# Optimization experiments

Hardware: AMD Instinct MI355X
Metric: run time of the kernel (lower is better)

Reference implementation:

```python
import jax, jax.numpy as jnp
import numpy as np

N_NODES = 50000
N_EDGES = 800000
IN_F = 32
HID = 64
N_LAYERS = 3
BN_EPS = 1e-5


def setup_inputs() -> dict:
    key = jax.random.key(0)
    ks = jax.random.split(key, 8)
    x = jax.random.normal(ks[0], (N_NODES, IN_F), dtype=jnp.float32)
    edge_index = jax.random.randint(ks[1], (2, N_EDGES), 0, N_NODES, dtype=jnp.int64)
    W_embed = jax.random.normal(ks[2], (IN_F, HID), dtype=jnp.float32) / np.sqrt(IN_F)
    b_embed = jnp.zeros((HID,), dtype=jnp.float32)
    W_convs = jax.random.normal(ks[3], (N_LAYERS, HID, HID), dtype=jnp.float32) / np.sqrt(HID)
    b_convs = jnp.zeros((N_LAYERS, HID), dtype=jnp.float32)
    bn_gamma = jnp.ones((HID,), dtype=jnp.float32)
    bn_beta = jnp.zeros((HID,), dtype=jnp.float32)
    return {"x": x, "edge_index": edge_index, "W_embed": W_embed, "b_embed": b_embed,
            "W_convs": W_convs, "b_convs": b_convs, "bn_gamma": bn_gamma, "bn_beta": bn_beta}


def _gcn_norm(edge_index, n_nodes):
    # PyG GCNConv: add self-loops, symmetric normalization deg^-1/2 * deg^-1/2
    loops = jnp.arange(n_nodes, dtype=edge_index.dtype)
    src = jnp.concatenate([edge_index[0], loops])
    dst = jnp.concatenate([edge_index[1], loops])
    deg = jax.ops.segment_sum(jnp.ones_like(dst, dtype=jnp.float32), dst, num_segments=n_nodes)
    dinv = jax.lax.rsqrt(jnp.maximum(deg, 1.0))
    norm = dinv[src] * dinv[dst]  # [E+N]
    return src, dst, norm


def reference(x, edge_index, W_embed, b_embed, W_convs, b_convs, bn_gamma, bn_beta):
    n = x.shape[0]
    src, dst, norm = _gcn_norm(edge_index, n)

    h = jax.nn.relu(x @ W_embed + b_embed)  # [N, HID]
    for l in range(N_LAYERS):
        res = h
        # GCNConv: linear transform, then normalized neighbor aggregation
        t = h @ W_convs[l] + b_convs[l]
        msg = t[src] * norm[:, None]                           # [E+N, HID]
        agg = jax.ops.segment_sum(msg, dst, num_segments=n)    # [N, HID]
        # BatchNorm1d (training-mode batch stats), shared across layers
        mu = jnp.mean(agg, axis=0)
        var = jnp.var(agg, axis=0)
        bn = (agg - mu) * jax.lax.rsqrt(var + BN_EPS) * bn_gamma + bn_beta
        h = jax.nn.relu(bn) + res
    return h
```

## Files before the change

kernel.cpp:

```cpp
#include <hip/hip_runtime.h>

#define IN_F 32
#define HID 64
#define N_LAYERS 3
#define BN_EPS 1e-5f

__device__ __forceinline__ unsigned short f2bf(float x) {
    unsigned u = __float_as_uint(x);
    u += 0x7fffu + ((u >> 16) & 1u);
    return (unsigned short)(u >> 16);
}
__device__ __forceinline__ float bflo(unsigned v) { return __uint_as_float(v << 16); }
__device__ __forceinline__ float bfhi(unsigned v) { return __uint_as_float(v & 0xffff0000u); }

__global__ __launch_bounds__(256) void k_zero(int* cnt, int* cursor, float* statsAll, int n) {
    int i = blockIdx.x * blockDim.x + threadIdx.x;
    if (i < n) cnt[i] = 0;
    if (i == 0) *cursor = 0;
    if (i < 2 * HID * N_LAYERS) statsAll[i] = 0.0f;
}

__global__ __launch_bounds__(256) void k_hist_rank(const int* __restrict__ dst, int* cnt,
                                                   unsigned short* __restrict__ rank, int e) {
    int i = blockIdx.x * blockDim.x + threadIdx.x;
    if (i >= e) return;
    int r = atomicAdd(&cnt[dst[i]], 1);
    rank[i] = (unsigned short)r;
}

__global__ __launch_bounds__(256) void k_assign(const int* __restrict__ cnt, int* rowbeg,
                                                float* dinv, int* cursor, int n) {
    int i = blockIdx.x * blockDim.x + threadIdx.x;
    int lane = threadIdx.x & 63;
    int c = (i < n) ? cnt[i] : 0;
    int s = c;
#pragma unroll
    for (int off = 1; off < 64; off <<= 1) {
        int t = __shfl_up(s, off, 64);
        if (lane >= off) s += t;
    }
    int total = __shfl(s, 63, 64);
    int base = 0;
    if (lane == 63) base = atomicAdd(cursor, total);
    base = __shfl(base, 63, 64);
    if (i < n) {
        rowbeg[i] = base + s - c;
        dinv[i] = rsqrtf((float)(c + 1));
    }
}

__global__ __launch_bounds__(256) void k_fill(const int* __restrict__ src,
                                              const int* __restrict__ dst,
                                              const int* __restrict__ rowbeg,
                                              const unsigned short* __restrict__ rank,
                                              unsigned short* __restrict__ csr_src, int e) {
    int i = blockIdx.x * blockDim.x + threadIdx.x;
    if (i >= e) return;
    int pos = rowbeg[dst[i]] + (int)rank[i];
    csr_src[pos] = (unsigned short)src[i];
}

__global__ __launch_bounds__(256) void k_embed_conv(const float* __restrict__ x,
                                                    const float* __restrict__ We,
                                                    const float* __restrict__ be,
                                                    const float* __restrict__ Wc,
                                                    const float* __restrict__ bc,
                                                    const float* __restrict__ dinv,
                                                    float* __restrict__ h,
                                                    unsigned short* __restrict__ t2b, int n) {
    __shared__ float sWe[IN_F * HID];
    __shared__ float sWc[HID * HID];
    __shared__ float sh[4][HID];
    for (int i = threadIdx.x; i < IN_F * HID; i += blockDim.x) sWe[i] = We[i];
    for (int i = threadIdx.x; i < HID * HID; i += blockDim.x) sWc[i] = Wc[i];
    __syncthreads();
    int f = threadIdx.x & 63;
    int wv = threadIdx.x >> 6;
    int plane = f >> 5, fin = f & 31;
    float bef = be[f], bcf = bc[f];
    int w0 = blockIdx.x * 4 + wv;
    int nw = gridDim.x * 4;
    for (int node = w0; node < n; node += nw) {
        const float* xr = x + (size_t)node * IN_F;
        float acc = bef;
#pragma unroll
        for (int k = 0; k < IN_F; ++k) acc = fmaf(xr[k], sWe[k * HID + f], acc);
        float hv = fmaxf(acc, 0.0f);
        h[(size_t)node * HID + f] = hv;
        sh[wv][f] = hv;
        float acc2 = bcf;
#pragma unroll
        for (int k4 = 0; k4 < HID / 4; ++k4) {
            float4 hv4 = ((const float4*)sh[wv])[k4];
            acc2 = fmaf(hv4.x, sWc[(k4 * 4 + 0) * HID + f], acc2);
            acc2 = fmaf(hv4.y, sWc[(k4 * 4 + 1) * HID + f], acc2);
            acc2 = fmaf(hv4.z, sWc[(k4 * 4 + 2) * HID + f], acc2);
            acc2 = fmaf(hv4.w, sWc[(k4 * 4 + 3) * HID + f], acc2);
        }
        t2b[(size_t)plane * n * 32 + (size_t)node * 32 + fin] = f2bf(acc2 * dinv[node]);
    }
}

__global__ __launch_bounds__(256) void k_bn_conv(const float* __restrict__ agg,
                                                 const float* __restrict__ stats,
                                                 const float* __restrict__ gamma,
                                                 const float* __restrict__ beta,
                                                 const float* __restrict__ W,
                                                 const float* __restrict__ b,
                                                 const float* __restrict__ dinv,
                                                 float* __restrict__ h,
                                                 unsigned short* __restrict__ t2b, int n, float invN) {
    __shared__ float sW[HID * HID];
    __shared__ float sh[4][HID];
    for (int i = threadIdx.x; i < HID * HID; i += blockDim.x) sW[i] = W[i];
    __syncthreads();
    int f = threadIdx.x & 63;
    int wv = threadIdx.x >> 6;
    int plane = f >> 5, fin = f & 31;
    float mu = stats[f] * invN;
    float var = fmaxf(stats[HID + f] * invN - mu * mu, 0.0f);
    float scale = rsqrtf(var + BN_EPS) * gamma[f];
    float shift = beta[f];
    float bf = b[f];
    int w0 = blockIdx.x * 4 + wv;
    int nw = gridDim.x * 4;
    for (int node = w0; node < n; node += nw) {
        size_t gid = (size_t)node * HID + f;
        float bnv = (agg[gid] - mu) * scale + shift;
        float hv = fmaxf(bnv, 0.0f) + h[gid];
        h[gid] = hv;
        sh[wv][f] = hv;
        float acc = bf;
#pragma unroll
        for (int k4 = 0; k4 < HID / 4; ++k4) {
            float4 hv4 = ((const float4*)sh[wv])[k4];
            acc = fmaf(hv4.x, sW[(k4 * 4 + 0) * HID + f], acc);
            acc = fmaf(hv4.y, sW[(k4 * 4 + 1) * HID + f], acc);
            acc = fmaf(hv4.z, sW[(k4 * 4 + 2) * HID + f], acc);
            acc = fmaf(hv4.w, sW[(k4 * 4 + 3) * HID + f], acc);
        }
        t2b[(size_t)plane * n * 32 + (size_t)node * 32 + fin] = f2bf(acc * dinv[node]);
    }
}

__global__ __launch_bounds__(256) void k_aggregate(const int* __restrict__ rowbeg,
                                                   const int* __restrict__ cnt,
                                                   const unsigned short* __restrict__ csr_src,
                                                   const unsigned short* __restrict__ t2b,
                                                   const float* __restrict__ dinv,
                                                   float* __restrict__ agg,
                                                   float* __restrict__ stats, int n) {
    __shared__ float lsum[HID], lsq[HID];
    if (threadIdx.x < HID) { lsum[threadIdx.x] = 0.0f; lsq[threadIdx.x] = 0.0f; }
    __syncthreads();

    const int plane = blockIdx.y;
    const unsigned short* tb = t2b + (size_t)plane * n * 32;

    int l4 = threadIdx.x & 3;
    int node = blockIdx.x * 64 + (threadIdx.x >> 2);

    float4 r0 = make_float4(0.f, 0.f, 0.f, 0.f);
    float4 r1 = make_float4(0.f, 0.f, 0.f, 0.f);

    if (node < n) {
        int beg = rowbeg[node], end = beg + cnt[node];
        uint4 sv = ((const uint4*)(tb + (size_t)node * 32))[l4];
        float4 a0, a1;
        a0.x = bflo(sv.x); a0.y = bfhi(sv.x); a0.z = bflo(sv.y); a0.w = bfhi(sv.y);
        a1.x = bflo(sv.z); a1.y = bfhi(sv.z); a1.z = bflo(sv.w); a1.w = bfhi(sv.w);
        int j = beg;
        for (; j + 8 <= end; j += 8) {
            int s0 = csr_src[j + 0], s1 = csr_src[j + 1];
            int s2 = csr_src[j + 2], s3 = csr_src[j + 3];
            int s4 = csr_src[j + 4], s5 = csr_src[j + 5];
            int s6 = csr_src[j + 6], s7 = csr_src[j + 7];
            uint4 v0 = ((const uint4*)(tb + (size_t)s0 * 32))[l4];
            uint4 v1 = ((const uint4*)(tb + (size_t)s1 * 32))[l4];
            uint4 v2 = ((const uint4*)(tb + (size_t)s2 * 32))[l4];
            uint4 v3 = ((const uint4*)(tb + (size_t)s3 * 32))[l4];
            uint4 v4 = ((const uint4*)(tb + (size_t)s4 * 32))[l4];
            uint4 v5 = ((const uint4*)(tb + (size_t)s5 * 32))[l4];
            uint4 v6 = ((const uint4*)(tb + (size_t)s6 * 32))[l4];
            uint4 v7 = ((const uint4*)(tb + (size_t)s7 * 32))[l4];
            a0.x += bflo(v0.x) + bflo(v1.x) + bflo(v2.x) + bflo(v3.x)
                  + bflo(v4.x) + bflo(v5.x) + bflo(v6.x) + bflo(v7.x);
            a0.y += bfhi(v0.x) + bfhi(v1.x) + bfhi(v2.x) + bfhi(v3.x)
                  + bfhi(v4.x) + bfhi(v5.x) + bfhi(v6.x) + bfhi(v7.x);
            a0.z += bflo(v0.y) + bflo(v1.y) + bflo(v2.y) + bflo(v3.y)
                  + bflo(v4.y) + bflo(v5.y) + bflo(v6.y) + bflo(v7.y);
            a0.w += bfhi(v0.y) + bfhi(v1.y) + bfhi(v2.y) + bfhi(v3.y)
                  + bfhi(v4.y) + bfhi(v5.y) + bfhi(v6.y) + bfhi(v7.y);
            a1.x += bflo(v0.z) + bflo(v1.z) + bflo(v2.z) + bflo(v3.z)
                  + bflo(v4.z) + bflo(v5.z) + bflo(v6.z) + bflo(v7.z);
            a1.y += bfhi(v0.z) + bfhi(v1.z) + bfhi(v2.z) + bfhi(v3.z)
                  + bfhi(v4.z) + bfhi(v5.z) + bfhi(v6.z) + bfhi(v7.z);
            a1.z += bflo(v0.w) + bflo(v1.w) + bflo(v2.w) + bflo(v3.w)
                  + bflo(v4.w) + bflo(v5.w) + bflo(v6.w) + bflo(v7.w);
            a1.w += bfhi(v0.w) + bfhi(v1.w) + bfhi(v2.w) + bfhi(v3.w)
                  + bfhi(v4.w) + bfhi(v5.w) + bfhi(v6.w) + bfhi(v7.w);
        }
        for (; j < end; ++j) {
            int s = csr_src[j];
            uint4 v = ((const uint4*)(tb + (size_t)s * 32))[l4];
            a0.x += bflo(v.x); a0.y += bfhi(v.x); a0.z += bflo(v.y); a0.w += bfhi(v.y);
            a1.x += bflo(v.z); a1.y += bfhi(v.z); a1.z += bflo(v.w); a1.w += bfhi(v.w);
        }
        float dv = dinv[node];
        r0.x = a0.x * dv; r0.y = a0.y * dv; r0.z = a0.z * dv; r0.w = a0.w * dv;
        r1.x = a1.x * dv; r1.y = a1.y * dv; r1.z = a1.z * dv; r1.w = a1.w * dv;
        float4* ar = (float4*)(agg + (size_t)node * HID + plane * 32);
        ar[l4 * 2 + 0] = r0;
        ar[l4 * 2 + 1] = r1;
    }

    float4 q0, q1;
    q0.x = r0.x * r0.x; q0.y = r0.y * r0.y; q0.z = r0.z * r0.z; q0.w = r0.w * r0.w;
    q1.x = r1.x * r1.x; q1.y = r1.y * r1.y; q1.z = r1.z * r1.z; q1.w = r1.w * r1.w;
#pragma unroll
    for (int off = 4; off < 64; off <<= 1) {
        r0.x += __shfl_xor(r0.x, off, 64); q0.x += __shfl_xor(q0.x, off, 64);
        r0.y += __shfl_xor(r0.y, off, 64); q0.y += __shfl_xor(q0.y, off, 64);
        r0.z += __shfl_xor(r0.z, off, 64); q0.z += __shfl_xor(q0.z, off, 64);
        r0.w += __shfl_xor(r0.w, off, 64); q0.w += __shfl_xor(q0.w, off, 64);
        r1.x += __shfl_xor(r1.x, off, 64); q1.x += __shfl_xor(q1.x, off, 64);
        r1.y += __shfl_xor(r1.y, off, 64); q1.y += __shfl_xor(q1.y, off, 64);
        r1.z += __shfl_xor(r1.z, off, 64); q1.z += __shfl_xor(q1.z, off, 64);
        r1.w += __shfl_xor(r1.w, off, 64); q1.w += __shfl_xor(q1.w, off, 64);
    }
    if ((threadIdx.x & 63) < 4) {
        int f0 = plane * 32 + l4 * 8;
        atomicAdd(&lsum[f0 + 0], r0.x); atomicAdd(&lsq[f0 + 0], q0.x);
        atomicAdd(&lsum[f0 + 1], r0.y); atomicAdd(&lsq[f0 + 1], q0.y);
        atomicAdd(&lsum[f0 + 2], r0.z); atomicAdd(&lsq[f0 + 2], q0.z);
        atomicAdd(&lsum[f0 + 3], r0.w); atomicAdd(&lsq[f0 + 3], q0.w);
        atomicAdd(&lsum[f0 + 4], r1.x); atomicAdd(&lsq[f0 + 4], q1.x);
        atomicAdd(&lsum[f0 + 5], r1.y); atomicAdd(&lsq[f0 + 5], q1.y);
        atomicAdd(&lsum[f0 + 6], r1.z); atomicAdd(&lsq[f0 + 6], q1.z);
        atomicAdd(&lsum[f0 + 7], r1.w); atomicAdd(&lsq[f0 + 7], q1.w);
    }
    __syncthreads();
    int fs = plane * 32 + (threadIdx.x & 31);
    if (threadIdx.x < 32) {
        atomicAdd(&stats[fs], lsum[fs]);
        atomicAdd(&stats[HID + fs], lsq[fs]);
    }
}

__global__ __launch_bounds__(256) void k_bn_apply(const float* __restrict__ agg,
                                                  const float* __restrict__ stats,
                                                  const float* __restrict__ gamma,
                                                  const float* __restrict__ beta,
                                                  float* __restrict__ h, int n, float invN) {
    int gid = blockIdx.x * blockDim.x + threadIdx.x;
    int node = gid >> 6, f = gid & 63;
    if (node >= n) return;
    float mu = stats[f] * invN;
    float var = fmaxf(stats[HID + f] * invN - mu * mu, 0.0f);
    float bn = (agg[gid] - mu) * rsqrtf(var + BN_EPS) * gamma[f] + beta[f];
    h[gid] = fmaxf(bn, 0.0f) + h[gid];
}

extern "C" void kernel_launch(void* const* d_in, const int* in_sizes, int n_in,
                              void* d_out, int out_size, void* d_ws, size_t ws_size,
                              hipStream_t stream) {
    const float* x       = (const float*)d_in[0];
    const int*   ei      = (const int*)d_in[1];
    const float* W_embed = (const float*)d_in[2];
    const float* b_embed = (const float*)d_in[3];
    const float* W_convs = (const float*)d_in[4];
    const float* b_convs = (const float*)d_in[5];
    const float* gamma   = (const float*)d_in[6];
    const float* beta    = (const float*)d_in[7];
    float* h = (float*)d_out;

    const int n = in_sizes[0] / IN_F;
    const int e = in_sizes[1] / 2;
    const int* src = ei;
    const int* dst = ei + e;

    unsigned short* t2b = (unsigned short*)d_ws;
    float* agg      = (float*)(t2b + (size_t)n * HID);
    float* dinv     = agg + (size_t)n * HID;
    float* statsAll = dinv + n;
    int*   rowbeg   = (int*)(statsAll + 2 * HID * N_LAYERS);
    int*   cnt      = rowbeg + n;
    int*   cursor   = cnt + n;
    unsigned short* csr_src = (unsigned short*)(cursor + 1);
    unsigned short* rank    = csr_src + e;

    const int nodeBlocks  = (n + 255) / 256;
    const int nfBlocks    = (n * HID + 255) / 256;
    const int edgeBlocks  = (e + 255) / 256;
    const dim3 aggGrid((n + 63) / 64, 2);
    const int embedBlocks = 1536;
    const int convBlocks  = 2048;

    k_zero<<<nodeBlocks, 256, 0, stream>>>(cnt, cursor, statsAll, n);
    k_hist_rank<<<edgeBlocks, 256, 0, stream>>>(dst, cnt, rank, e);
    k_assign<<<nodeBlocks, 256, 0, stream>>>(cnt, rowbeg, dinv, cursor, n);
    k_fill<<<edgeBlocks, 256, 0, stream>>>(src, dst, rowbeg, rank, csr_src, e);

    const float invN = 1.0f / (float)n;

    k_embed_conv<<<embedBlocks, 256, 0, stream>>>(x, W_embed, b_embed, W_convs, b_convs,
                                                  dinv, h, t2b, n);

    for (int l = 0; l < N_LAYERS; ++l) {
        float* stats = statsAll + (size_t)l * 2 * HID;
        k_aggregate<<<aggGrid, 256, 0, stream>>>(rowbeg, cnt, csr_src, t2b, dinv,
                                                 agg, stats, n);
        if (l < N_LAYERS - 1) {
            const float* Wl = W_convs + (size_t)(l + 1) * HID * HID;
            const float* bl = b_convs + (size_t)(l + 1) * HID;
            k_bn_conv<<<convBlocks, 256, 0, stream>>>(agg, stats, gamma, beta, Wl, bl, dinv,
                                                      h, t2b, n, invN);
        } else {
            k_bn_apply<<<nfBlocks, 256, 0, stream>>>(agg, stats, gamma, beta, h, n, invN);
        }
    }
}
```

Baseline: 270.9 us.

## Use wave shuffles for node matvecs, prefetch next node, interleave aggregate planes

The embed and BN+conv kernels now broadcast each node's activations with wave shuffles instead of staging them in shared memory. Each kernel also prefetches the next node's inputs (x, agg, h, dinv) one iteration ahead and splits the dot products across four accumulators to shorten the dependency chains. The aggregate kernel moves from a 2D grid to a 1D grid that interleaves the two feature planes, so blocks that read the same nodes run close together and can share cache. This raises register use a little and relies on the 32/64-width shuffles being cheaper than the LDS round trip.

Result: slower. 340.6 us (+25.7%).

```diff
diff --git a/kernel.cpp b/kernel.cpp
--- a/kernel.cpp
+++ b/kernel.cpp
@@ -70,7 +70,6 @@
                                                     unsigned short* __restrict__ t2b, int n) {
     __shared__ float sWe[IN_F * HID];
     __shared__ float sWc[HID * HID];
-    __shared__ float sh[4][HID];
     for (int i = threadIdx.x; i < IN_F * HID; i += blockDim.x) sWe[i] = We[i];
     for (int i = threadIdx.x; i < HID * HID; i += blockDim.x) sWc[i] = Wc[i];
     __syncthreads();
@@ -78,26 +77,40 @@
     int wv = threadIdx.x >> 6;
     int plane = f >> 5, fin = f & 31;
     float bef = be[f], bcf = bc[f];
-    int w0 = blockIdx.x * 4 + wv;
     int nw = gridDim.x * 4;
-    for (int node = w0; node < n; node += nw) {
-        const float* xr = x + (size_t)node * IN_F;
-        float acc = bef;
-#pragma unroll
-        for (int k = 0; k < IN_F; ++k) acc = fmaf(xr[k], sWe[k * HID + f], acc);
-        float hv = fmaxf(acc, 0.0f);
+    int node = blockIdx.x * 4 + wv;
+
+    float xv = (node < n) ? x[(size_t)node * IN_F + (f & 31)] : 0.0f;
+    float dv = (node < n) ? dinv[node] : 0.0f;
+
+    while (node < n) {
+        int nxt = node + nw;
+        float xv_n = (nxt < n) ? x[(size_t)nxt * IN_F + (f & 31)] : 0.0f;
+        float dv_n = (nxt < n) ? dinv[nxt] : 0.0f;
+
+        float a0 = bef, a1 = 0.f, a2 = 0.f, a3 = 0.f;
+#pragma unroll
+        for (int k = 0; k < IN_F; k += 4) {
+            a0 = fmaf(__shfl(xv, k + 0, 32), sWe[(k + 0) * HID + f], a0);
+            a1 = fmaf(__shfl(xv, k + 1, 32), sWe[(k + 1) * HID + f], a1);
+            a2 = fmaf(__shfl(xv, k + 2, 32), sWe[(k + 2) * HID + f], a2);
+            a3 = fmaf(__shfl(xv, k + 3, 32), sWe[(k + 3) * HID + f], a3);
+        }
+        float hv = fmaxf((a0 + a1) + (a2 + a3), 0.0f);
         h[(size_t)node * HID + f] = hv;
-        sh[wv][f] = hv;
-        float acc2 = bcf;
-#pragma unroll
-        for (int k4 = 0; k4 < HID / 4; ++k4) {
-            float4 hv4 = ((const float4*)sh[wv])[k4];
-            acc2 = fmaf(hv4.x, sWc[(k4 * 4 + 0) * HID + f], acc2);
-            acc2 = fmaf(hv4.y, sWc[(k4 * 4 + 1) * HID + f], acc2);
-            acc2 = fmaf(hv4.z, sWc[(k4 * 4 + 2) * HID + f], acc2);
-            acc2 = fmaf(hv4.w, sWc[(k4 * 4 + 3) * HID + f], acc2);
-        }
-        t2b[(size_t)plane * n * 32 + (size_t)node * 32 + fin] = f2bf(acc2 * dinv[node]);
+
+        float c0 = bcf, c1 = 0.f, c2 = 0.f, c3 = 0.f;
+#pragma unroll
+        for (int k = 0; k < HID; k += 4) {
+            c0 = fmaf(__shfl(hv, k + 0, 64), sWc[(k + 0) * HID + f], c0);
+            c1 = fmaf(__shfl(hv, k + 1, 64), sWc[(k + 1) * HID + f], c1);
+            c2 = fmaf(__shfl(hv, k + 2, 64), sWc[(k + 2) * HID + f], c2);
+            c3 = fmaf(__shfl(hv, k + 3, 64), sWc[(k + 3) * HID + f], c3);
+        }
+        float t = ((c0 + c1) + (c2 + c3)) * dv;
+        t2b[(size_t)plane * n * 32 + (size_t)node * 32 + fin] = f2bf(t);
+
+        node = nxt; xv = xv_n; dv = dv_n;
     }
 }
 
@@ -111,7 +124,6 @@
                                                  float* __restrict__ h,
                                                  unsigned short* __restrict__ t2b, int n, float invN) {
     __shared__ float sW[HID * HID];
-    __shared__ float sh[4][HID];
     for (int i = threadIdx.x; i < HID * HID; i += blockDim.x) sW[i] = W[i];
     __syncthreads();
     int f = threadIdx.x & 63;
@@ -122,24 +134,39 @@
     float scale = rsqrtf(var + BN_EPS) * gamma[f];
     float shift = beta[f];
     float bf = b[f];
-    int w0 = blockIdx.x * 4 + wv;
     int nw = gridDim.x * 4;
-    for (int node = w0; node < n; node += nw) {
+    int node = blockIdx.x * 4 + wv;
+
+    float av = 0.f, hold = 0.f, dv = 0.f;
+    if (node < n) {
         size_t gid = (size_t)node * HID + f;
-        float bnv = (agg[gid] - mu) * scale + shift;
-        float hv = fmaxf(bnv, 0.0f) + h[gid];
-        h[gid] = hv;
-        sh[wv][f] = hv;
-        float acc = bf;
-#pragma unroll
-        for (int k4 = 0; k4 < HID / 4; ++k4) {
-            float4 hv4 = ((const float4*)sh[wv])[k4];
-            acc = fmaf(hv4.x, sW[(k4 * 4 + 0) * HID + f], acc);
-            acc = fmaf(hv4.y, sW[(k4 * 4 + 1) * HID + f], acc);
-            acc = fmaf(hv4.z, sW[(k4 * 4 + 2) * HID + f], acc);
-            acc = fmaf(hv4.w, sW[(k4 * 4 + 3) * HID + f], acc);
-        }
-        t2b[(size_t)plane * n * 32 + (size_t)node * 32 + fin] = f2bf(acc * dinv[node]);
+        av = agg[gid]; hold = h[gid]; dv = dinv[node];
+    }
+
+    while (node < n) {
+        int nxt = node + nw;
+        float av_n = 0.f, hold_n = 0.f, dv_n = 0.f;
+        if (nxt < n) {
+            size_t gid_n = (size_t)nxt * HID + f;
+            av_n = agg[gid_n]; hold_n = h[gid_n]; dv_n = dinv[nxt];
+        }
+
+        float bnv = (av - mu) * scale + shift;
+        float hv = fmaxf(bnv, 0.0f) + hold;
+        h[(size_t)node * HID + f] = hv;
+
+        float c0 = bf, c1 = 0.f, c2 = 0.f, c3 = 0.f;
+#pragma unroll
+        for (int k = 0; k < HID; k += 4) {
+            c0 = fmaf(__shfl(hv, k + 0, 64), sW[(k + 0) * HID + f], c0);
+            c1 = fmaf(__shfl(hv, k + 1, 64), sW[(k + 1) * HID + f], c1);
+            c2 = fmaf(__shfl(hv, k + 2, 64), sW[(k + 2) * HID + f], c2);
+            c3 = fmaf(__shfl(hv, k + 3, 64), sW[(k + 3) * HID + f], c3);
+        }
+        float t = ((c0 + c1) + (c2 + c3)) * dv;
+        t2b[(size_t)plane * n * 32 + (size_t)node * 32 + fin] = f2bf(t);
+
+        node = nxt; av = av_n; hold = hold_n; dv = dv_n;
     }
 }
 
@@ -154,11 +181,11 @@
     if (threadIdx.x < HID) { lsum[threadIdx.x] = 0.0f; lsq[threadIdx.x] = 0.0f; }
     __syncthreads();
 
-    const int plane = blockIdx.y;
+    const int plane = blockIdx.x & 1;
     const unsigned short* tb = t2b + (size_t)plane * n * 32;
 
     int l4 = threadIdx.x & 3;
-    int node = blockIdx.x * 64 + (threadIdx.x >> 2);
+    int node = (blockIdx.x >> 1) * 64 + (threadIdx.x >> 2);
 
     float4 r0 = make_float4(0.f, 0.f, 0.f, 0.f);
     float4 r1 = make_float4(0.f, 0.f, 0.f, 0.f);
@@ -292,7 +319,7 @@
     const int nodeBlocks  = (n + 255) / 256;
     const int nfBlocks    = (n * HID + 255) / 256;
     const int edgeBlocks  = (e + 255) / 256;
-    const dim3 aggGrid((n + 63) / 64, 2);
+    const int aggBlocks   = ((n + 63) / 64) * 2;
     const int embedBlocks = 1536;
     const int convBlocks  = 2048;
 
@@ -308,8 +335,8 @@
 
     for (int l = 0; l < N_LAYERS; ++l) {
         float* stats = statsAll + (size_t)l * 2 * HID;
-        k_aggregate<<<aggGrid, 256, 0, stream>>>(rowbeg, cnt, csr_src, t2b, dinv,
-                                                 agg, stats, n);
+        k_aggregate<<<aggBlocks, 256, 0, stream>>>(rowbeg, cnt, csr_src, t2b, dinv,
+                                                   agg, stats, n);
         if (l < N_LAYERS - 1) {
             const float* Wl = W_convs + (size_t)(l + 1) * HID * HID;
             const float* bl = b_convs + (size_t)(l + 1) * HID;
```

## Register-block dense transforms over 8 nodes per wavefront and interleave aggregate planes

Applied to the files above, without the earlier changes.

The embed and conv kernels now process 8 nodes at a time per wavefront, so each weight read from shared memory feeds 8 FMAs held in register accumulators instead of 1. The grid is sized so each wavefront handles exactly 16 nodes, and x rows are staged cooperatively through LDS with float4 loads. The aggregate kernel folds the two feature planes into blockIdx.x so adjacent blocks work on the same nodes' planes, which may improve cache locality for the shared csr reads. The cost is more registers and more LDS per block, which could lower occupancy.

New measurement: 358.9 us. 32.5% more time.

```diff
diff --git a/kernel.cpp b/kernel.cpp
--- a/kernel.cpp
+++ b/kernel.cpp
@@ -70,34 +70,77 @@
                                                     unsigned short* __restrict__ t2b, int n) {
     __shared__ float sWe[IN_F * HID];
     __shared__ float sWc[HID * HID];
-    __shared__ float sh[4][HID];
+    __shared__ float shx[4][8][IN_F];
+    __shared__ float shh[4][8 * HID];
     for (int i = threadIdx.x; i < IN_F * HID; i += blockDim.x) sWe[i] = We[i];
     for (int i = threadIdx.x; i < HID * HID; i += blockDim.x) sWc[i] = Wc[i];
     __syncthreads();
+
     int f = threadIdx.x & 63;
     int wv = threadIdx.x >> 6;
     int plane = f >> 5, fin = f & 31;
     float bef = be[f], bcf = bc[f];
-    int w0 = blockIdx.x * 4 + wv;
-    int nw = gridDim.x * 4;
-    for (int node = w0; node < n; node += nw) {
-        const float* xr = x + (size_t)node * IN_F;
-        float acc = bef;
-#pragma unroll
-        for (int k = 0; k < IN_F; ++k) acc = fmaf(xr[k], sWe[k * HID + f], acc);
-        float hv = fmaxf(acc, 0.0f);
-        h[(size_t)node * HID + f] = hv;
-        sh[wv][f] = hv;
-        float acc2 = bcf;
+    int ml = f >> 3, sub = f & 7;
+    int wgid = blockIdx.x * 4 + wv;
+
+    for (int iter = 0; iter < 2; ++iter) {
+        int base = wgid * 16 + iter * 8;
+        if (base >= n) break;
+
+        int xnode = base + ml;
+        float4 xv = (xnode < n) ? ((const float4*)(x + (size_t)xnode * IN_F))[sub]
+                                : make_float4(0.f, 0.f, 0.f, 0.f);
+        ((float4*)&shx[wv][ml][0])[sub] = xv;
+
+        float acc[8];
+#pragma unroll
+        for (int m = 0; m < 8; ++m) acc[m] = bef;
+#pragma unroll
+        for (int k4 = 0; k4 < IN_F / 4; ++k4) {
+            float w0 = sWe[(k4 * 4 + 0) * HID + f];
+            float w1 = sWe[(k4 * 4 + 1) * HID + f];
+            float w2 = sWe[(k4 * 4 + 2) * HID + f];
+            float w3 = sWe[(k4 * 4 + 3) * HID + f];
+#pragma unroll
+            for (int m = 0; m < 8; ++m) {
+                float4 xq = ((const float4*)&shx[wv][m][0])[k4];
+                acc[m] = fmaf(xq.x, w0, acc[m]);
+                acc[m] = fmaf(xq.y, w1, acc[m]);
+                acc[m] = fmaf(xq.z, w2, acc[m]);
+                acc[m] = fmaf(xq.w, w3, acc[m]);
+            }
+        }
+#pragma unroll
+        for (int m = 0; m < 8; ++m) {
+            float hv = fmaxf(acc[m], 0.0f);
+            int node = base + m;
+            if (node < n) h[(size_t)node * HID + f] = hv;
+            shh[wv][m * HID + f] = hv;
+        }
+
+#pragma unroll
+        for (int m = 0; m < 8; ++m) acc[m] = bcf;
 #pragma unroll
         for (int k4 = 0; k4 < HID / 4; ++k4) {
-            float4 hv4 = ((const float4*)sh[wv])[k4];
-            acc2 = fmaf(hv4.x, sWc[(k4 * 4 + 0) * HID + f], acc2);
-            acc2 = fmaf(hv4.y, sWc[(k4 * 4 + 1) * HID + f], acc2);
-            acc2 = fmaf(hv4.z, sWc[(k4 * 4 + 2) * HID + f], acc2);
-            acc2 = fmaf(hv4.w, sWc[(k4 * 4 + 3) * HID + f], acc2);
-        }
-        t2b[(size_t)plane * n * 32 + (size_t)node * 32 + fin] = f2bf(acc2 * dinv[node]);
+            float w0 = sWc[(k4 * 4 + 0) * HID + f];
+            float w1 = sWc[(k4 * 4 + 1) * HID + f];
+            float w2 = sWc[(k4 * 4 + 2) * HID + f];
+            float w3 = sWc[(k4 * 4 + 3) * HID + f];
+#pragma unroll
+            for (int m = 0; m < 8; ++m) {
+                float4 hq = ((const float4*)&shh[wv][m * HID])[k4];
+                acc[m] = fmaf(hq.x, w0, acc[m]);
+                acc[m] = fmaf(hq.y, w1, acc[m]);
+                acc[m] = fmaf(hq.z, w2, acc[m]);
+                acc[m] = fmaf(hq.w, w3, acc[m]);
+            }
+        }
+#pragma unroll
+        for (int m = 0; m < 8; ++m) {
+            int node = base + m;
+            if (node < n)
+                t2b[(size_t)plane * n * 32 + (size_t)node * 32 + fin] = f2bf(acc[m] * dinv[node]);
+        }
     }
 }
 
@@ -111,9 +154,10 @@
                                                  float* __restrict__ h,
                                                  unsigned short* __restrict__ t2b, int n, float invN) {
     __shared__ float sW[HID * HID];
-    __shared__ float sh[4][HID];
+    __shared__ float shh[4][8 * HID];
     for (int i = threadIdx.x; i < HID * HID; i += blockDim.x) sW[i] = W[i];
     __syncthreads();
+
     int f = threadIdx.x & 63;
     int wv = threadIdx.x >> 6;
     int plane = f >> 5, fin = f & 31;
@@ -122,24 +166,52 @@
     float scale = rsqrtf(var + BN_EPS) * gamma[f];
     float shift = beta[f];
     float bf = b[f];
-    int w0 = blockIdx.x * 4 + wv;
-    int nw = gridDim.x * 4;
-    for (int node = w0; node < n; node += nw) {
-        size_t gid = (size_t)node * HID + f;
-        float bnv = (agg[gid] - mu) * scale + shift;
-        float hv = fmaxf(bnv, 0.0f) + h[gid];
-        h[gid] = hv;
-        sh[wv][f] = hv;
-        float acc = bf;
+    int wgid = blockIdx.x * 4 + wv;
+
+    for (int iter = 0; iter < 2; ++iter) {
+        int base = wgid * 16 + iter * 8;
+        if (base >= n) break;
+
+        float av[8], hold[8];
+#pragma unroll
+        for (int m = 0; m < 8; ++m) {
+            int node = base + m;
+            if (node < n) {
+                size_t gid = (size_t)node * HID + f;
+                av[m] = agg[gid]; hold[m] = h[gid];
+            } else { av[m] = 0.f; hold[m] = 0.f; }
+        }
+        float acc[8];
+#pragma unroll
+        for (int m = 0; m < 8; ++m) {
+            float bnv = (av[m] - mu) * scale + shift;
+            float hv = fmaxf(bnv, 0.0f) + hold[m];
+            int node = base + m;
+            if (node < n) h[(size_t)node * HID + f] = hv;
+            shh[wv][m * HID + f] = hv;
+            acc[m] = bf;
+        }
 #pragma unroll
         for (int k4 = 0; k4 < HID / 4; ++k4) {
-            float4 hv4 = ((const float4*)sh[wv])[k4];
-            acc = fmaf(hv4.x, sW[(k4 * 4 + 0) * HID + f], acc);
-            acc = fmaf(hv4.y, sW[(k4 * 4 + 1) * HID + f], acc);
-            acc = fmaf(hv4.z, sW[(k4 * 4 + 2) * HID + f], acc);
-            acc = fmaf(hv4.w, sW[(k4 * 4 + 3) * HID + f], acc);
-        }
-        t2b[(size_t)plane * n * 32 + (size_t)node * 32 + fin] = f2bf(acc * dinv[node]);
+            float w0 = sW[(k4 * 4 + 0) * HID + f];
+            float w1 = sW[(k4 * 4 + 1) * HID + f];
+            float w2 = sW[(k4 * 4 + 2) * HID + f];
+            float w3 = sW[(k4 * 4 + 3) * HID + f];
+#pragma unroll
+            for (int m = 0; m < 8; ++m) {
+                float4 hq = ((const float4*)&shh[wv][m * HID])[k4];
+                acc[m] = fmaf(hq.x, w0, acc[m]);
+                acc[m] = fmaf(hq.y, w1, acc[m]);
+                acc[m] = fmaf(hq.z, w2, acc[m]);
+                acc[m] = fmaf(hq.w, w3, acc[m]);
+            }
+        }
+#pragma unroll
+        for (int m = 0; m < 8; ++m) {
+            int node = base + m;
+            if (node < n)
+                t2b[(size_t)plane * n * 32 + (size_t)node * 32 + fin] = f2bf(acc[m] * dinv[node]);
+        }
     }
 }
 
@@ -154,11 +226,11 @@
     if (threadIdx.x < HID) { lsum[threadIdx.x] = 0.0f; lsq[threadIdx.x] = 0.0f; }
     __syncthreads();
 
-    const int plane = blockIdx.y;
+    const int plane = blockIdx.x & 1;
     const unsigned short* tb = t2b + (size_t)plane * n * 32;
 
     int l4 = threadIdx.x & 3;
-    int node = blockIdx.x * 64 + (threadIdx.x >> 2);
+    int node = (blockIdx.x >> 1) * 64 + (threadIdx.x >> 2);
 
     float4 r0 = make_float4(0.f, 0.f, 0.f, 0.f);
     float4 r1 = make_float4(0.f, 0.f, 0.f, 0.f);
@@ -292,9 +364,8 @@
     const int nodeBlocks  = (n + 255) / 256;
     const int nfBlocks    = (n * HID + 255) / 256;
     const int edgeBlocks  = (e + 255) / 256;
-    const dim3 aggGrid((n + 63) / 64, 2);
-    const int embedBlocks = 1536;
-    const int convBlocks  = 2048;
+    const int aggBlocks   = ((n + 63) / 64) * 2;
+    const int denseBlocks = (n + 16 * 4 - 1) / (16 * 4);
 
     k_zero<<<nodeBlocks, 256, 0, stream>>>(cnt, cursor, statsAll, n);
     k_hist_rank<<<edgeBlocks, 256, 0, stream>>>(dst, cnt, rank, e);
@@ -303,18 +374,18 @@
 
     const float invN = 1.0f / (float)n;
 
-    k_embed_conv<<<embedBlocks, 256, 0, stream>>>(x, W_embed, b_embed, W_convs, b_convs,
+    k_embed_conv<<<denseBlocks, 256, 0, stream>>>(x, W_embed, b_embed, W_convs, b_convs,
                                                   dinv, h, t2b, n);
 
     for (int l = 0; l < N_LAYERS; ++l) {
         float* stats = statsAll + (size_t)l * 2 * HID;
-        k_aggregate<<<aggGrid, 256, 0, stream>>>(rowbeg, cnt, csr_src, t2b, dinv,
-                                                 agg, stats, n);
+        k_aggregate<<<aggBlocks, 256, 0, stream>>>(rowbeg, cnt, csr_src, t2b, dinv,
+                                                   agg, stats, n);
         if (l < N_LAYERS - 1) {
             const float* Wl = W_convs + (size_t)(l + 1) * HID * HID;
             const float* bl = b_convs + (size_t)(l + 1) * HID;
-            k_bn_conv<<<convBlocks, 256, 0, stream>>>(agg, stats, gamma, beta, Wl, bl, dinv,
-                                                      h, t2b, n, invN);
+            k_bn_conv<<<denseBlocks, 256, 0, stream>>>(agg, stats, gamma, beta, Wl, bl, dinv,
+                                                       h, t2b, n, invN);
         } else {
             k_bn_apply<<<nfBlocks, 256, 0, stream>>>(agg, stats, gamma, beta, h, n, invN);
         }
```
